# Performance work log

Hardware: AMD Instinct MI355X
Metric: run time of the kernel (lower is better)

Reference implementation:

```python
import jax, jax.numpy as jnp
import numpy as np

VOCAB, EMB, OUT = 32000, 1024, 10
B, S = 64, 512

def setup_inputs() -> dict:
    key = jax.random.key(0)
    k1, k2, k3, k4, k5, k6, k7 = jax.random.split(key, 7)
    x = jax.random.randint(k1, (B, S), 0, VOCAB)
    label = jax.random.randint(k2, (B,), 0, OUT)
    emb_table = jax.random.normal(k3, (VOCAB, EMB), dtype=jnp.float32) * 0.02
    W = jax.random.normal(k4, (EMB, EMB), dtype=jnp.float32) / np.sqrt(EMB)
    b = jax.random.normal(k5, (EMB,), dtype=jnp.float32) * 0.01
    Wc = jax.random.normal(k6, (OUT, EMB), dtype=jnp.float32) / np.sqrt(EMB)
    bc = jax.random.normal(k7, (OUT,), dtype=jnp.float32) * 0.01
    return {"x": x, "label": label, "emb_table": emb_table, "W": W, "b": b, "Wc": Wc, "bc": bc}

def reference(x, label, emb_table, W, b, Wc, bc):
    # embedding lookup: (B, S, EMB)
    emb = emb_table[x]
    # affine recurrence h_i = W @ (h_{i-1} + x_i) + b, h_{-1} = 0
    def step(h, xi):
        h = (h + xi) @ W.T + b  # (B, EMB)
        return h, h
    h0 = jnp.zeros((emb.shape[0], emb.shape[2]), dtype=emb.dtype)
    _, hs = jax.lax.scan(step, h0, jnp.swapaxes(emb, 0, 1))  # hs: (S, B, EMB)
    result = jnp.swapaxes(hs, 0, 1)  # (B, S, EMB)
    pred = result @ Wc.T + bc  # (B, S, OUT)
    pred_mean = jnp.mean(pred, axis=1)  # (B, OUT)
    # cross entropy (mean reduction)
    logp = jax.nn.log_softmax(pred_mean, axis=-1)
    loss = -jnp.mean(jnp.take_along_axis(logp, label[:, None], axis=-1))
    return loss
```

## Files before the change

kernel.cpp:

```cpp
#include <hip/hip_runtime.h>

#define OFF_C    0L
#define OFF_CS   5636096L
#define OFF_WP   5718016L
#define OFF_BS   5799936L
#define OFF_PRED 5810176L
#define OFF_PART 5810816L
#define OFF_U16  6138496L
#define UQAH 0L
#define UQAL 1048576L
#define UQATH 2097152L
#define UQATL 3145728L
#define UQBH 4194304L
#define UQBL 5242880L
#define UQBTH 6291456L
#define UQBTL 7340032L
#define URH  8388608L
#define URL  13631488L
#define CS4  1409024L
#define CS2  2621440L

typedef unsigned short u16;
typedef unsigned int u32;
typedef u16 us8 __attribute__((ext_vector_type(8)));
typedef short s8v __attribute__((ext_vector_type(8)));
typedef float f4v __attribute__((ext_vector_type(4)));

__device__ __forceinline__ u16 f2b(float f) {
    u32 u = __float_as_uint(f);
    return (u16)((u + 0x7fffu + ((u >> 16) & 1u)) >> 16);
}
__device__ __forceinline__ float b2f(u16 h) {
    return __uint_as_float((u32)h << 16);
}

__global__ __launch_bounds__(256) void split_w(
    const float* __restrict__ W, u16* __restrict__ Qh, u16* __restrict__ Ql,
    u16* __restrict__ QTh, u16* __restrict__ QTl)
{
    __shared__ u32 T[64][65];
    const int tid = threadIdx.x;
    const int r = tid >> 2, c0 = (tid & 3) << 4;
    alignas(16) u16 h[16], l[16];
    const size_t src = (size_t)(blockIdx.y * 64 + r) * 1024 + blockIdx.x * 64 + c0;
    #pragma unroll
    for (int q = 0; q < 4; q++) {
        float4 v = *(const float4*)(W + src + q * 4);
        float vv[4] = {v.x, v.y, v.z, v.w};
        #pragma unroll
        for (int i = 0; i < 4; i++) {
            u16 hh = f2b(vv[i]);
            u16 ll = f2b(vv[i] - b2f(hh));
            h[q * 4 + i] = hh; l[q * 4 + i] = ll;
            T[c0 + q * 4 + i][r] = ((u32)ll << 16) | hh;
        }
    }
    *(us8*)(Qh + src) = *(const us8*)&h[0];
    *(us8*)(Qh + src + 8) = *(const us8*)&h[8];
    *(us8*)(Ql + src) = *(const us8*)&l[0];
    *(us8*)(Ql + src + 8) = *(const us8*)&l[8];
    __syncthreads();
    alignas(16) u16 th[16], tl[16];
    #pragma unroll
    for (int i = 0; i < 16; i++) {
        u32 v = T[r][c0 + i];
        th[i] = (u16)(v & 0xffffu); tl[i] = (u16)(v >> 16);
    }
    const size_t dst = (size_t)(blockIdx.x * 64 + r) * 1024 + blockIdx.y * 64 + c0;
    *(us8*)(QTh + dst) = *(const us8*)&th[0];
    *(us8*)(QTh + dst + 8) = *(const us8*)&th[8];
    *(us8*)(QTl + dst) = *(const us8*)&tl[0];
    *(us8*)(QTl + dst + 8) = *(const us8*)&tl[8];
}

__global__ __launch_bounds__(256) void thin_d0(
    const float* __restrict__ Wc, const float* __restrict__ W, float* __restrict__ pbuf)
{
    const int o = blockIdx.x >> 2;
    const int d = ((blockIdx.x & 3) << 8) + threadIdx.x;
    const int k0 = blockIdx.y << 7;
    float acc = 0.f;
    #pragma unroll 8
    for (int k = k0; k < k0 + 128; k++)
        acc = fmaf(Wc[o * 1024 + k], W[(size_t)k * 1024 + d], acc);
    pbuf[(size_t)blockIdx.y * 10240 + o * 1024 + d] = acc;
}

__global__ __launch_bounds__(256) void d0_fin(
    const float* __restrict__ pbuf, u16* __restrict__ Rh, u16* __restrict__ Rl)
{
    const int od = blockIdx.x * 256 + threadIdx.x;
    float v = 0.f;
    #pragma unroll
    for (int z = 0; z < 8; z++) v += pbuf[(size_t)z * 10240 + od];
    u16 h = f2b(v);
    Rh[od] = h;
    Rl[od] = f2b(v - b2f(h));
}

__global__ __launch_bounds__(256) void gemm_mfma(
    const u16* __restrict__ Ah_g, const u16* __restrict__ Al_g,
    const u16* __restrict__ Rh_g, const u16* __restrict__ Rl_g,
    const u16* __restrict__ BTh_g, const u16* __restrict__ BTl_g,
    float* __restrict__ C, int a1M, int a2M, int kc, long cS)
{
    const int M = a1M + a2M;
    __shared__ alignas(16) u16 Ash[4][129][8], Asl[4][129][8];
    __shared__ alignas(16) u16 Bsh[4][129][8], Bsl[4][129][8];
    const int tid = threadIdx.x;
    const int bn = blockIdx.x << 7, bm = blockIdx.y << 7;
    const int kstart = blockIdx.z * kc, kend = kstart + kc;
    const int lane = tid & 63, wid = tid >> 6;
    const int wm = (wid & 1) << 6, wn = (wid >> 1) << 6;
    const int lrow = lane & 15, kq = lane >> 4;
    const int srow = tid >> 1;
    const int skq = (tid & 1) << 1;
    const int sk = skq << 3;

    const int gmA = bm + srow;
    const bool aval = (gmA < M);
    const u16* pAh; const u16* pAl;
    if (gmA < a1M) {
        pAh = Ah_g + (size_t)gmA * 1024;
        pAl = Al_g + (size_t)gmA * 1024;
    } else {
        int rr = aval ? (gmA - a1M) : 0;
        pAh = Rh_g + (size_t)rr * 1024;
        pAl = Rl_g + (size_t)rr * 1024;
    }
    const u16* pBh = BTh_g + (size_t)(bn + srow) * 1024;
    const u16* pBl = BTl_g + (size_t)(bn + srow) * 1024;

    f4v acc[4][4];
    #pragma unroll
    for (int i = 0; i < 4; i++)
        #pragma unroll
        for (int j = 0; j < 4; j++) acc[i][j] = 0.f;

    us8 ah0, ah1, al0, al1, bh0, bh1, bl0, bl1;
    auto loadstep = [&](int k) {
        if (aval) {
            ah0 = *(const us8*)(pAh + k + sk); ah1 = *(const us8*)(pAh + k + sk + 8);
            al0 = *(const us8*)(pAl + k + sk); al1 = *(const us8*)(pAl + k + sk + 8);
        } else { ah0 = 0; ah1 = 0; al0 = 0; al1 = 0; }
        bh0 = *(const us8*)(pBh + k + sk); bh1 = *(const us8*)(pBh + k + sk + 8);
        bl0 = *(const us8*)(pBl + k + sk); bl1 = *(const us8*)(pBl + k + sk + 8);
    };
    loadstep(kstart);

    for (int k0 = kstart; k0 < kend; k0 += 32) {
        *(us8*)&Ash[skq][srow][0] = ah0;
        *(us8*)&Ash[skq + 1][srow][0] = ah1;
        *(us8*)&Asl[skq][srow][0] = al0;
        *(us8*)&Asl[skq + 1][srow][0] = al1;
        *(us8*)&Bsh[skq][srow][0] = bh0;
        *(us8*)&Bsh[skq + 1][srow][0] = bh1;
        *(us8*)&Bsl[skq][srow][0] = bl0;
        *(us8*)&Bsl[skq + 1][srow][0] = bl1;
        __syncthreads();
        if (k0 + 32 < kend) loadstep(k0 + 32);
        s8v afh[4], afl[4], bfh[4], bfl[4];
        #pragma unroll
        for (int i = 0; i < 4; i++) {
            afh[i] = *(const s8v*)&Ash[kq][wm + (i << 4) + lrow][0];
            afl[i] = *(const s8v*)&Asl[kq][wm + (i << 4) + lrow][0];
            bfh[i] = *(const s8v*)&Bsh[kq][wn + (i << 4) + lrow][0];
            bfl[i] = *(const s8v*)&Bsl[kq][wn + (i << 4) + lrow][0];
        }
        #pragma unroll
        for (int mi = 0; mi < 4; mi++)
            #pragma unroll
            for (int ni = 0; ni < 4; ni++) {
                acc[mi][ni] = __builtin_amdgcn_mfma_f32_16x16x32_bf16(
                    afh[mi], bfh[ni], acc[mi][ni], 0, 0, 0);
                acc[mi][ni] = __builtin_amdgcn_mfma_f32_16x16x32_bf16(
                    afl[mi], bfh[ni], acc[mi][ni], 0, 0, 0);
                acc[mi][ni] = __builtin_amdgcn_mfma_f32_16x16x32_bf16(
                    afh[mi], bfl[ni], acc[mi][ni], 0, 0, 0);
            }
        __syncthreads();
    }
    float* Cz = C + (size_t)blockIdx.z * cS;
    #pragma unroll
    for (int mi = 0; mi < 4; mi++)
        #pragma unroll
        for (int i = 0; i < 4; i++) {
            const int gr = bm + wm + (mi << 4) + (kq << 2) + i;
            if (gr >= M) continue;
            #pragma unroll
            for (int ni = 0; ni < 4; ni++)
                Cz[(size_t)gr * 1024 + bn + wn + (ni << 4) + lrow] = acc[mi][ni][i];
        }
}

__global__ __launch_bounds__(256) void combine(
    const float* __restrict__ C, int zsplit, long cS, int a1M, int a2M, int M,
    u16* __restrict__ Qh, u16* __restrict__ Ql,
    u16* __restrict__ QTh, u16* __restrict__ QTl,
    u16* __restrict__ Rh, u16* __restrict__ Rl)
{
    __shared__ u32 T[64][65];
    const int tid = threadIdx.x;
    const int r = tid >> 2, c0 = (tid & 3) << 4;
    const int row0 = blockIdx.y << 6, col0 = blockIdx.x << 6;
    const int gr = row0 + r;
    const bool isQ = (row0 < a1M);
    alignas(16) u16 h[16], l[16];
    #pragma unroll
    for (int q = 0; q < 4; q++) {
        float4 v = make_float4(0.f, 0.f, 0.f, 0.f);
        if (gr < M) {
            const float* p = C + (size_t)gr * 1024 + col0 + c0 + q * 4;
            v = *(const float4*)p;
            for (int z = 1; z < zsplit; z++) {
                float4 t = *(const float4*)(p + (size_t)z * cS);
                v.x += t.x; v.y += t.y; v.z += t.z; v.w += t.w;
            }
        }
        float vv[4] = {v.x, v.y, v.z, v.w};
        #pragma unroll
        for (int i = 0; i < 4; i++) {
            u16 hh = f2b(vv[i]);
            u16 ll = f2b(vv[i] - b2f(hh));
            h[q * 4 + i] = hh; l[q * 4 + i] = ll;
            if (isQ) T[c0 + q * 4 + i][r] = ((u32)ll << 16) | hh;
        }
    }
    if (isQ) {
        const size_t dst = (size_t)gr * 1024 + col0 + c0;
        *(us8*)(Qh + dst) = *(const us8*)&h[0];
        *(us8*)(Qh + dst + 8) = *(const us8*)&h[8];
        *(us8*)(Ql + dst) = *(const us8*)&l[0];
        *(us8*)(Ql + dst + 8) = *(const us8*)&l[8];
        __syncthreads();
        alignas(16) u16 th[16], tl[16];
        #pragma unroll
        for (int i = 0; i < 16; i++) {
            u32 v = T[r][c0 + i];
            th[i] = (u16)(v & 0xffffu); tl[i] = (u16)(v >> 16);
        }
        const size_t dt = (size_t)(col0 + r) * 1024 + row0 + c0;
        *(us8*)(QTh + dt) = *(const us8*)&th[0];
        *(us8*)(QTh + dt + 8) = *(const us8*)&th[8];
        *(us8*)(QTl + dt) = *(const us8*)&tl[0];
        *(us8*)(QTl + dt + 8) = *(const us8*)&tl[8];
    } else if (gr < M) {
        const size_t dst = (size_t)(gr - a1M + a2M) * 1024 + col0 + c0;
        *(us8*)(Rh + dst) = *(const us8*)&h[0];
        *(us8*)(Rh + dst + 8) = *(const us8*)&h[8];
        *(us8*)(Rl + dst) = *(const us8*)&l[0];
        *(us8*)(Rl + dst + 8) = *(const us8*)&l[8];
    }
}

__global__ __launch_bounds__(256) void prefix_pass1(
    const u16* __restrict__ Rh, const u16* __restrict__ Rl,
    float* __restrict__ csum, float* __restrict__ wpart)
{
    const int od = blockIdx.x * 256 + threadIdx.x;
    const int c = blockIdx.y;
    const u16* ph = Rh + (size_t)(c * 64) * 10240 + od;
    const u16* pl = Rl + (size_t)(c * 64) * 10240 + od;
    float cs = 0.f, wsv = 0.f;
    #pragma unroll 4
    for (int i = 0; i < 64; i++) {
        float v = b2f(ph[(size_t)i * 10240]) + b2f(pl[(size_t)i * 10240]);
        cs += v;
        wsv += (float)(511 - (c * 64 + i)) * v;
    }
    csum[c * 10240 + od] = cs;
    wpart[c * 10240 + od] = wsv;
}

__global__ __launch_bounds__(256) void prefix_pass2(
    const u16* __restrict__ Rh, const u16* __restrict__ Rl,
    const float* __restrict__ csum, float* __restrict__ Acc)
{
    const int od = blockIdx.x * 256 + threadIdx.x;
    const int c = blockIdx.y;
    float run = 0.f;
    #pragma unroll
    for (int c2 = 0; c2 < 8; c2++) {
        float t = csum[c2 * 10240 + od];
        run += (c2 < c) ? t : 0.f;
    }
    const u16* ph = Rh + (size_t)(c * 64) * 10240 + od;
    const u16* pl = Rl + (size_t)(c * 64) * 10240 + od;
    float* pa = Acc + (size_t)(c * 64) * 10240 + od;
    #pragma unroll 4
    for (int i = 0; i < 64; i++) {
        run += b2f(ph[(size_t)i * 10240]) + b2f(pl[(size_t)i * 10240]);
        pa[(size_t)i * 10240] = run;
    }
}

__global__ __launch_bounds__(256) void bsum_k(
    const float* __restrict__ wpart, const float* __restrict__ Wc, float* __restrict__ bsum)
{
    const int od = blockIdx.x * 256 + threadIdx.x;
    float s = 512.f * Wc[od];
    #pragma unroll
    for (int c = 0; c < 8; c++) s += wpart[c * 10240 + od];
    bsum[od] = s;
}

__global__ __launch_bounds__(256) void contract_k(
    const float* __restrict__ Acc, const int* __restrict__ x,
    const float* __restrict__ emb, float* __restrict__ part)
{
    __shared__ float As[10240];
    const int tid = threadIdx.x;
    const int j = blockIdx.x, bg = blockIdx.y;
    const int w = tid >> 6, lane = tid & 63;
    const int b0 = (bg << 4) + (w << 2);
    const float4* emb4 = (const float4*)emb;
    const int i0 = x[(b0 + 0) * 512 + j], i1 = x[(b0 + 1) * 512 + j];
    const int i2 = x[(b0 + 2) * 512 + j], i3 = x[(b0 + 3) * 512 + j];
    float4 e0[4], e1[4], e2[4], e3[4];
    #pragma unroll
    for (int c = 0; c < 4; c++) {
        e0[c] = emb4[(size_t)i0 * 256 + (c << 6) + lane];
        e1[c] = emb4[(size_t)i1 * 256 + (c << 6) + lane];
        e2[c] = emb4[(size_t)i2 * 256 + (c << 6) + lane];
        e3[c] = emb4[(size_t)i3 * 256 + (c << 6) + lane];
    }
    const float4* Ap = (const float4*)(Acc + (size_t)(511 - j) * 10240);
    float4* As4 = (float4*)As;
    #pragma unroll
    for (int i = 0; i < 10; i++) As4[tid + (i << 8)] = Ap[tid + (i << 8)];
    __syncthreads();

    float p0[10], p1[10], p2[10], p3[10];
    #pragma unroll
    for (int o = 0; o < 10; o++) {
        float s0 = 0.f, s1 = 0.f, s2 = 0.f, s3 = 0.f;
        #pragma unroll
        for (int c = 0; c < 4; c++) {
            float4 a = As4[(o << 8) + (c << 6) + lane];
            s0 = fmaf(a.x, e0[c].x, s0); s0 = fmaf(a.y, e0[c].y, s0);
            s0 = fmaf(a.z, e0[c].z, s0); s0 = fmaf(a.w, e0[c].w, s0);
            s1 = fmaf(a.x, e1[c].x, s1); s1 = fmaf(a.y, e1[c].y, s1);
            s1 = fmaf(a.z, e1[c].z, s1); s1 = fmaf(a.w, e1[c].w, s1);
            s2 = fmaf(a.x, e2[c].x, s2); s2 = fmaf(a.y, e2[c].y, s2);
            s2 = fmaf(a.z, e2[c].z, s2); s2 = fmaf(a.w, e2[c].w, s2);
            s3 = fmaf(a.x, e3[c].x, s3); s3 = fmaf(a.y, e3[c].y, s3);
            s3 = fmaf(a.z, e3[c].z, s3); s3 = fmaf(a.w, e3[c].w, s3);
        }
        p0[o] = s0; p1[o] = s1; p2[o] = s2; p3[o] = s3;
    }
    #pragma unroll
    for (int o = 0; o < 10; o++) {
        #pragma unroll
        for (int off = 32; off; off >>= 1) {
            p0[o] += __shfl_down(p0[o], off);
            p1[o] += __shfl_down(p1[o], off);
            p2[o] += __shfl_down(p2[o], off);
            p3[o] += __shfl_down(p3[o], off);
        }
    }
    if (lane == 0) {
        float* pp = part + (size_t)j * 640 + b0 * 10;
        #pragma unroll
        for (int o = 0; o < 10; o++) {
            pp[o] = p0[o]; pp[10 + o] = p1[o];
            pp[20 + o] = p2[o]; pp[30 + o] = p3[o];
        }
    }
}

__global__ __launch_bounds__(256) void reduce_part(
    const float* __restrict__ part, float* __restrict__ pred)
{
    const int gid = blockIdx.x * 256 + threadIdx.x;
    const int out = gid >> 4, s = gid & 15;
    float p = 0.f;
    #pragma unroll 8
    for (int t = 0; t < 32; t++) p += part[(size_t)(s + (t << 4)) * 640 + out];
    for (int off = 8; off; off >>= 1) p += __shfl_down(p, off, 16);
    if (s == 0) pred[out] = p;
}

__global__ __launch_bounds__(640) void finalize_k(
    const float* __restrict__ pred, const float* __restrict__ bsum,
    const float* __restrict__ bvec, const float* __restrict__ bc,
    const int* __restrict__ label, float* __restrict__ out)
{
    __shared__ float biasv[10];
    const int tid = threadIdx.x;
    {
        int o = tid >> 6, lane = tid & 63;
        float s = 0.f;
        for (int k = lane; k < 1024; k += 64) s = fmaf(bsum[o * 1024 + k], bvec[k], s);
        for (int off = 32; off; off >>= 1) s += __shfl_down(s, off, 64);
        if (lane == 0) biasv[o] = s;
    }
    __syncthreads();
    if (tid < 64) {
        int b = tid, lab = label[b];
        float v[10], mx = -1e30f;
        #pragma unroll
        for (int o = 0; o < 10; o++) {
            v[o] = (pred[b * 10 + o] + biasv[o]) * (1.f / 512.f) + bc[o];
            mx = fmaxf(mx, v[o]);
        }
        float se = 0.f, vl = 0.f;
        #pragma unroll
        for (int o = 0; o < 10; o++) {
            se += __expf(v[o] - mx);
            if (o == lab) vl = v[o];
        }
        float myloss = (mx + __logf(se)) - vl;
        for (int off = 32; off; off >>= 1) myloss += __shfl_down(myloss, off, 64);
        if (tid == 0) out[0] = myloss * (1.f / 64.f);
    }
}

extern "C" void kernel_launch(void* const* d_in, const int* in_sizes, int n_in,
                              void* d_out, int out_size, void* d_ws, size_t ws_size,
                              hipStream_t stream) {
    const int*   x     = (const int*)d_in[0];
    const int*   label = (const int*)d_in[1];
    const float* emb   = (const float*)d_in[2];
    const float* W     = (const float*)d_in[3];
    const float* bvec  = (const float*)d_in[4];
    const float* Wc    = (const float*)d_in[5];
    const float* bc    = (const float*)d_in[6];
    float* ws    = (float*)d_ws;
    float* C     = ws + OFF_C;
    float* Acc   = ws + OFF_C;
    float* csum  = ws + OFF_CS;
    float* wpart = ws + OFF_WP;
    float* bsum  = ws + OFF_BS;
    float* pred  = ws + OFF_PRED;
    float* part  = ws + OFF_PART;
    u16*   ub    = (u16*)(ws + OFF_U16);
    u16* RH = ub + URH;
    u16* RL = ub + URL;
    u16* qin[4]  = {ub + UQAH, ub + UQAL, ub + UQATH, ub + UQATL};
    u16* qout[4] = {ub + UQBH, ub + UQBL, ub + UQBTH, ub + UQBTL};
    float* out   = (float*)d_out;

    split_w<<<dim3(16, 16), 256, 0, stream>>>(W, qin[0], qin[1], qin[2], qin[3]);
    thin_d0<<<dim3(40, 8), 256, 0, stream>>>(Wc, W, C);
    d0_fin<<<40, 256, 0, stream>>>(C, RH, RL);

    int a2M = 10;
    for (int k = 2; k <= 10; k++) {
        const int a1M = (k < 10) ? 1024 : 0;
        const int M = a1M + a2M;
        const int zs = (M <= 1376) ? 4 : 2;
        const long cS = (zs == 4) ? CS4 : CS2;
        const int kc = 1024 / zs;
        dim3 g(8, (M + 127) / 128, zs);
        gemm_mfma<<<g, 256, 0, stream>>>(qin[0], qin[1], RH, RL, qin[2], qin[3],
                                         C, a1M, a2M, kc, cS);
        combine<<<dim3(16, (M + 63) / 64), 256, 0, stream>>>(
            C, zs, cS, a1M, a2M, M,
            qout[0], qout[1], qout[2], qout[3], RH, RL);
        for (int i = 0; i < 4; i++) { u16* t = qin[i]; qin[i] = qout[i]; qout[i] = t; }
        a2M <<= 1;
    }

    prefix_pass1<<<dim3(40, 8), 256, 0, stream>>>(RH, RL, csum, wpart);
    prefix_pass2<<<dim3(40, 8), 256, 0, stream>>>(RH, RL, csum, Acc);
    bsum_k<<<40, 256, 0, stream>>>(wpart, Wc, bsum);
    contract_k<<<dim3(512, 4), 256, 0, stream>>>(Acc, x, emb, part);
    reduce_part<<<40, 256, 0, stream>>>(part, pred);
    finalize_k<<<1, 640, 0, stream>>>(pred, bsum, bvec, bc, label, out);
}
```

Before: 522.3 us.

## Double split-K depth in GEMM chain and reuse Acc tile across batch chunks

The split-K factor for the repeated-squaring MFMA GEMMs doubles (8 or 4 instead of 4 or 2), and the workspace offsets grow to hold the larger partial buffer. This adds parallelism for the small-M GEMMs at the cost of more partial-sum traffic in combine. contract_k now launches one block per timestep instead of four. Each block loads the 40KB Acc tile into LDS once and loops over four batch chunks, prefetching the next chunk's embedding rows before the shuffle reduction. This removes redundant Acc loads but reduces grid parallelism.

```diff
diff --git a/kernel.cpp b/kernel.cpp
--- a/kernel.cpp
+++ b/kernel.cpp
@@ -1,12 +1,12 @@
 #include <hip/hip_runtime.h>
 
 #define OFF_C    0L
-#define OFF_CS   5636096L
-#define OFF_WP   5718016L
-#define OFF_BS   5799936L
-#define OFF_PRED 5810176L
-#define OFF_PART 5810816L
-#define OFF_U16  6138496L
+#define OFF_CS   11272192L
+#define OFF_WP   11354112L
+#define OFF_BS   11436032L
+#define OFF_PRED 11446272L
+#define OFF_PART 11446912L
+#define OFF_U16  11774592L
 #define UQAH 0L
 #define UQAL 1048576L
 #define UQATH 2097152L
@@ -17,8 +17,8 @@
 #define UQBTL 7340032L
 #define URH  8388608L
 #define URL  13631488L
-#define CS4  1409024L
-#define CS2  2621440L
+#define CS8  1409024L
+#define CS4  2621440L
 
 typedef unsigned short u16;
 typedef unsigned int u32;
@@ -310,12 +310,14 @@
 {
     __shared__ float As[10240];
     const int tid = threadIdx.x;
-    const int j = blockIdx.x, bg = blockIdx.y;
+    const int j = blockIdx.x;
     const int w = tid >> 6, lane = tid & 63;
-    const int b0 = (bg << 4) + (w << 2);
     const float4* emb4 = (const float4*)emb;
-    const int i0 = x[(b0 + 0) * 512 + j], i1 = x[(b0 + 1) * 512 + j];
-    const int i2 = x[(b0 + 2) * 512 + j], i3 = x[(b0 + 3) * 512 + j];
+    float4* As4 = (float4*)As;
+    const float4* Ap = (const float4*)(Acc + (size_t)(511 - j) * 10240);
+
+    int i0 = x[((w << 2) + 0) * 512 + j], i1 = x[((w << 2) + 1) * 512 + j];
+    int i2 = x[((w << 2) + 2) * 512 + j], i3 = x[((w << 2) + 3) * 512 + j];
     float4 e0[4], e1[4], e2[4], e3[4];
     #pragma unroll
     for (int c = 0; c < 4; c++) {
@@ -324,46 +326,59 @@
         e2[c] = emb4[(size_t)i2 * 256 + (c << 6) + lane];
         e3[c] = emb4[(size_t)i3 * 256 + (c << 6) + lane];
     }
-    const float4* Ap = (const float4*)(Acc + (size_t)(511 - j) * 10240);
-    float4* As4 = (float4*)As;
     #pragma unroll
     for (int i = 0; i < 10; i++) As4[tid + (i << 8)] = Ap[tid + (i << 8)];
     __syncthreads();
 
-    float p0[10], p1[10], p2[10], p3[10];
-    #pragma unroll
-    for (int o = 0; o < 10; o++) {
-        float s0 = 0.f, s1 = 0.f, s2 = 0.f, s3 = 0.f;
-        #pragma unroll
-        for (int c = 0; c < 4; c++) {
-            float4 a = As4[(o << 8) + (c << 6) + lane];
-            s0 = fmaf(a.x, e0[c].x, s0); s0 = fmaf(a.y, e0[c].y, s0);
-            s0 = fmaf(a.z, e0[c].z, s0); s0 = fmaf(a.w, e0[c].w, s0);
-            s1 = fmaf(a.x, e1[c].x, s1); s1 = fmaf(a.y, e1[c].y, s1);
-            s1 = fmaf(a.z, e1[c].z, s1); s1 = fmaf(a.w, e1[c].w, s1);
-            s2 = fmaf(a.x, e2[c].x, s2); s2 = fmaf(a.y, e2[c].y, s2);
-            s2 = fmaf(a.z, e2[c].z, s2); s2 = fmaf(a.w, e2[c].w, s2);
-            s3 = fmaf(a.x, e3[c].x, s3); s3 = fmaf(a.y, e3[c].y, s3);
-            s3 = fmaf(a.z, e3[c].z, s3); s3 = fmaf(a.w, e3[c].w, s3);
-        }
-        p0[o] = s0; p1[o] = s1; p2[o] = s2; p3[o] = s3;
-    }
-    #pragma unroll
-    for (int o = 0; o < 10; o++) {
-        #pragma unroll
-        for (int off = 32; off; off >>= 1) {
-            p0[o] += __shfl_down(p0[o], off);
-            p1[o] += __shfl_down(p1[o], off);
-            p2[o] += __shfl_down(p2[o], off);
-            p3[o] += __shfl_down(p3[o], off);
-        }
-    }
-    if (lane == 0) {
-        float* pp = part + (size_t)j * 640 + b0 * 10;
+    for (int chunk = 0; chunk < 4; chunk++) {
+        float p0[10], p1[10], p2[10], p3[10];
         #pragma unroll
         for (int o = 0; o < 10; o++) {
-            pp[o] = p0[o]; pp[10 + o] = p1[o];
-            pp[20 + o] = p2[o]; pp[30 + o] = p3[o];
+            float s0 = 0.f, s1 = 0.f, s2 = 0.f, s3 = 0.f;
+            #pragma unroll
+            for (int c = 0; c < 4; c++) {
+                float4 a = As4[(o << 8) + (c << 6) + lane];
+                s0 = fmaf(a.x, e0[c].x, s0); s0 = fmaf(a.y, e0[c].y, s0);
+                s0 = fmaf(a.z, e0[c].z, s0); s0 = fmaf(a.w, e0[c].w, s0);
+                s1 = fmaf(a.x, e1[c].x, s1); s1 = fmaf(a.y, e1[c].y, s1);
+                s1 = fmaf(a.z, e1[c].z, s1); s1 = fmaf(a.w, e1[c].w, s1);
+                s2 = fmaf(a.x, e2[c].x, s2); s2 = fmaf(a.y, e2[c].y, s2);
+                s2 = fmaf(a.z, e2[c].z, s2); s2 = fmaf(a.w, e2[c].w, s2);
+                s3 = fmaf(a.x, e3[c].x, s3); s3 = fmaf(a.y, e3[c].y, s3);
+                s3 = fmaf(a.z, e3[c].z, s3); s3 = fmaf(a.w, e3[c].w, s3);
+            }
+            p0[o] = s0; p1[o] = s1; p2[o] = s2; p3[o] = s3;
+        }
+        if (chunk < 3) {
+            const int bn = ((chunk + 1) << 4) + (w << 2);
+            i0 = x[(bn + 0) * 512 + j]; i1 = x[(bn + 1) * 512 + j];
+            i2 = x[(bn + 2) * 512 + j]; i3 = x[(bn + 3) * 512 + j];
+            #pragma unroll
+            for (int c = 0; c < 4; c++) {
+                e0[c] = emb4[(size_t)i0 * 256 + (c << 6) + lane];
+                e1[c] = emb4[(size_t)i1 * 256 + (c << 6) + lane];
+                e2[c] = emb4[(size_t)i2 * 256 + (c << 6) + lane];
+                e3[c] = emb4[(size_t)i3 * 256 + (c << 6) + lane];
+            }
+        }
+        #pragma unroll
+        for (int o = 0; o < 10; o++) {
+            #pragma unroll
+            for (int off = 32; off; off >>= 1) {
+                p0[o] += __shfl_down(p0[o], off);
+                p1[o] += __shfl_down(p1[o], off);
+                p2[o] += __shfl_down(p2[o], off);
+                p3[o] += __shfl_down(p3[o], off);
+            }
+        }
+        if (lane == 0) {
+            const int bbase = (chunk << 4) + (w << 2);
+            float* pp = part + (size_t)j * 640 + bbase * 10;
+            #pragma unroll
+            for (int o = 0; o < 10; o++) {
+                pp[o] = p0[o]; pp[10 + o] = p1[o];
+                pp[20 + o] = p2[o]; pp[30 + o] = p3[o];
+            }
         }
     }
 }
@@ -448,8 +463,8 @@
     for (int k = 2; k <= 10; k++) {
         const int a1M = (k < 10) ? 1024 : 0;
         const int M = a1M + a2M;
-        const int zs = (M <= 1376) ? 4 : 2;
-        const long cS = (zs == 4) ? CS4 : CS2;
+        const int zs = (M <= 1376) ? 8 : 4;
+        const long cS = (zs == 8) ? CS8 : CS4;
         const int kc = 1024 / zs;
         dim3 g(8, (M + 127) / 128, zs);
         gemm_mfma<<<g, 256, 0, stream>>>(qin[0], qin[1], RH, RL, qin[2], qin[3],
@@ -464,7 +479,7 @@
     prefix_pass1<<<dim3(40, 8), 256, 0, stream>>>(RH, RL, csum, wpart);
     prefix_pass2<<<dim3(40, 8), 256, 0, stream>>>(RH, RL, csum, Acc);
     bsum_k<<<40, 256, 0, stream>>>(wpart, Wc, bsum);
-    contract_k<<<dim3(512, 4), 256, 0, stream>>>(Acc, x, emb, part);
+    contract_k<<<512, 256, 0, stream>>>(Acc, x, emb, part);
     reduce_part<<<40, 256, 0, stream>>>(part, pred);
     finalize_k<<<1, 640, 0, stream>>>(pred, bsum, bvec, bc, label, out);
 }
```

Measured after the change: 584.0 us. 11.8% more time.
